# Kernel optimization log

Measured on AMD Instinct MI355X. Metric: run time of the kernel, lower is better.

Reference implementation:

```python
import jax, jax.numpy as jnp
import numpy as np

N = 50000; E = 800000; IN = 64; HID = 128; H = 8; C = 16; G = 64
NEG = 0.2  # leaky_relu negative slope (GATv2 default and explicit in forward)

def _ln(x, g, b, eps=1e-5):
    mu = jnp.mean(x, -1, keepdims=True)
    var = jnp.var(x, -1, keepdims=True)
    return (x - mu) * jax.lax.rsqrt(var + eps) * g + b

def _prelu(x, a):
    return jnp.where(x >= 0, x, a * x)

def _gatv2(h, src, dst, Wl, bl, Wr, br, att, bias):
    # GATv2Conv: heads=H, out=C per head, concat=True, add_self_loops=True
    n = h.shape[0]
    loop = jnp.arange(n, dtype=src.dtype)
    s = jnp.concatenate([src, loop]); d = jnp.concatenate([dst, loop])
    xl = (h @ Wl + bl).reshape(n, H, C)   # source transform (messages)
    xr = (h @ Wr + br).reshape(n, H, C)   # target transform
    z = jax.nn.leaky_relu(xl[s] + xr[d], NEG)          # [Etot,H,C]
    e = jnp.einsum('ehc,hc->eh', z, att)               # [Etot,H]
    m = jax.ops.segment_max(e, d, num_segments=n)      # scatter-softmax over dst
    w = jnp.exp(e - m[d])
    denom = jax.ops.segment_sum(w, d, num_segments=n)
    alpha = w / (denom[d] + 1e-16)
    out = jax.ops.segment_sum(xl[s] * alpha[:, :, None], d, num_segments=n)
    return out.reshape(n, H * C) + bias

def _sage(h, src, dst, Wp, bp, Wl, bl, Wr):
    # SAGEConv(aggr='mean', normalize=True, project=True)
    n = h.shape[0]
    xp = jax.nn.relu(h @ Wp + bp)                      # project before aggregation
    summ = jax.ops.segment_sum(xp[src], dst, num_segments=n)
    cnt = jax.ops.segment_sum(jnp.ones_like(dst, dtype=h.dtype), dst, num_segments=n)
    mean = summ / jnp.maximum(cnt, 1.0)[:, None]
    out = mean @ Wl + bl + h @ Wr                      # root uses un-projected h
    nrm = jnp.linalg.norm(out, axis=-1, keepdims=True)
    return out / jnp.maximum(nrm, 1e-12)               # F.normalize(p=2, dim=-1)

def _forward(x, W_in, b_in, W_res, b_res,
             g0_Wl, g0_bl, g0_Wr, g0_br, g0_att, g0_bias,
             s1_Wp, s1_bp, s1_Wl, s1_bl, s1_Wr,
             g2_Wl, g2_bl, g2_Wr, g2_br, g2_att, g2_bias,
             s3_Wp, s3_bp, s3_Wl, s3_bl, s3_Wr,
             ln_g, ln_b, Wap, bap,
             Wc1, bc1, a1, Wc2, bc2, a2, Wc3, bc3,
             edge_index, batch):
    src, dst = edge_index[0], edge_index[1]
    h = (x @ W_in + b_in) + (x @ W_res + b_res)        # input_proj + res_proj
    xs0 = jax.nn.elu(_ln(_gatv2(h, src, dst, g0_Wl, g0_bl, g0_Wr, g0_br, g0_att, g0_bias), ln_g[0], ln_b[0]))
    xs1 = jax.nn.leaky_relu(_ln(_sage(xs0, src, dst, s1_Wp, s1_bp, s1_Wl, s1_bl, s1_Wr), ln_g[1], ln_b[1]), NEG)
    xs2 = jax.nn.elu(_ln(_gatv2(xs1, src, dst, g2_Wl, g2_bl, g2_Wr, g2_br, g2_att, g2_bias), ln_g[2], ln_b[2]))
    xs3 = jax.nn.leaky_relu(_ln(_sage(xs2, src, dst, s3_Wp, s3_bp, s3_Wl, s3_bl, s3_Wr), ln_g[3], ln_b[3]), NEG)
    h = jnp.maximum(jnp.maximum(xs0, xs1), jnp.maximum(xs2, xs3))  # JumpingKnowledge('max')
    att = jax.nn.sigmoid(h @ Wap + bap)
    h = h * att
    summ = jax.ops.segment_sum(h, batch, num_segments=G)
    cnt = jax.ops.segment_sum(jnp.ones((h.shape[0],), h.dtype), batch, num_segments=G)
    pooled = summ / jnp.maximum(cnt, 1.0)[:, None]     # global_mean_pool
    z = _prelu(pooled @ Wc1 + bc1, a1)
    z = _prelu(z @ Wc2 + bc2, a2)
    return z @ Wc3 + bc3

def setup_inputs():
    key = jax.random.key(0)
    ks = iter(jax.random.split(key, 64))
    def nrm(shape, fan):
        return jax.random.normal(next(ks), shape, jnp.float32) / np.sqrt(fan).astype(np.float32)
    inp = {}
    inp['x'] = jax.random.normal(next(ks), (N, IN), jnp.float32)
    inp['edge_index'] = jax.random.randint(next(ks), (2, E), 0, N, jnp.int32)
    inp['batch'] = jnp.sort(jax.random.randint(next(ks), (N,), 0, G, jnp.int32))
    inp['W_in'] = nrm((IN, HID), IN); inp['b_in'] = jnp.zeros((HID,))
    inp['W_res'] = nrm((IN, HID), IN); inp['b_res'] = jnp.zeros((HID,))
    for p in ('g0', 'g2'):
        inp[p + '_Wl'] = nrm((HID, HID), HID); inp[p + '_bl'] = jnp.zeros((HID,))
        inp[p + '_Wr'] = nrm((HID, HID), HID); inp[p + '_br'] = jnp.zeros((HID,))
        inp[p + '_att'] = nrm((H, C), C); inp[p + '_bias'] = jnp.zeros((HID,))
    for p in ('s1', 's3'):
        inp[p + '_Wp'] = nrm((HID, HID), HID); inp[p + '_bp'] = jnp.zeros((HID,))
        inp[p + '_Wl'] = nrm((HID, HID), HID); inp[p + '_bl'] = jnp.zeros((HID,))
        inp[p + '_Wr'] = nrm((HID, HID), HID)
    inp['ln_g'] = jnp.ones((4, HID)); inp['ln_b'] = jnp.zeros((4, HID))
    inp['Wap'] = nrm((HID, 1), HID); inp['bap'] = jnp.zeros((1,))
    inp['Wc1'] = nrm((HID, HID), HID); inp['bc1'] = jnp.zeros((HID,))
    inp['a1'] = jnp.float32(0.25)
    inp['Wc2'] = nrm((HID, HID // 2), HID); inp['bc2'] = jnp.zeros((HID // 2,))
    inp['a2'] = jnp.float32(0.25)
    inp['Wc3'] = nrm((HID // 2, 2), HID // 2); inp['bc3'] = jnp.zeros((2,))
    return inp

def reference(x, edge_index, batch, W_in, b_in, W_res, b_res,
              g0_Wl, g0_bl, g0_Wr, g0_br, g0_att, g0_bias,
              s1_Wp, s1_bp, s1_Wl, s1_bl, s1_Wr,
              g2_Wl, g2_bl, g2_Wr, g2_br, g2_att, g2_bias,
              s3_Wp, s3_bp, s3_Wl, s3_bl, s3_Wr,
              ln_g, ln_b, Wap, bap, Wc1, bc1, a1, Wc2, bc2, a2, Wc3, bc3):
    return _forward(x, W_in, b_in, W_res, b_res,
                    g0_Wl, g0_bl, g0_Wr, g0_br, g0_att, g0_bias,
                    s1_Wp, s1_bp, s1_Wl, s1_bl, s1_Wr,
                    g2_Wl, g2_bl, g2_Wr, g2_br, g2_att, g2_bias,
                    s3_Wp, s3_bp, s3_Wl, s3_bl, s3_Wr,
                    ln_g, ln_b, Wap, bap, Wc1, bc1, a1, Wc2, bc2, a2, Wc3, bc3,
                    edge_index, batch)
```

## Files before the change

kernel.cpp:

```cpp
#include <hip/hip_runtime.h>
#include <math.h>

constexpr int N_ = 50000;
constexpr int E_ = 800000;
constexpr int IN_ = 64;
constexpr int HID_ = 128;
constexpr int G_ = 64;
constexpr float NEG_ = 0.2f;
constexpr float LOG2E_ = 1.44269504088896340736f;

#define ACT_NONE 0
#define ACT_RELU 1

typedef _Float16 half8 __attribute__((ext_vector_type(8)));
typedef _Float16 half2v __attribute__((ext_vector_type(2)));
typedef float floatx4 __attribute__((ext_vector_type(4)));

__global__ __launch_bounds__(256) void hist_kernel(const int* __restrict__ dst,
                                                   int* __restrict__ deg, int e) {
  int i = blockIdx.x * 256 + threadIdx.x;
  if (i < e) atomicAdd(&deg[dst[i]], 1);
}

__global__ __launch_bounds__(256) void scan1_kernel(const int* __restrict__ deg,
                                                    int* __restrict__ excl,
                                                    int* __restrict__ bscan, int n) {
  __shared__ int sh[256];
  int t = threadIdx.x;
  int i = blockIdx.x * 256 + t;
  int v = (i < n) ? deg[i] : 0;
  sh[t] = v;
  __syncthreads();
  for (int off = 1; off < 256; off <<= 1) {
    int y = (t >= off) ? sh[t - off] : 0;
    __syncthreads();
    sh[t] += y;
    __syncthreads();
  }
  int incl = sh[t];
  if (i < n) excl[i] = incl - v;
  if (t == 255) bscan[blockIdx.x] = incl;
}

__global__ __launch_bounds__(256) void scan2_kernel(int* __restrict__ data, int nb) {
  __shared__ int sh[256];
  int t = threadIdx.x;
  int v = (t < nb) ? data[t] : 0;
  sh[t] = v;
  __syncthreads();
  for (int off = 1; off < 256; off <<= 1) {
    int y = (t >= off) ? sh[t - off] : 0;
    __syncthreads();
    sh[t] += y;
    __syncthreads();
  }
  if (t < nb) data[t] = sh[t] - v;
}

__global__ __launch_bounds__(256) void scan3_kernel(int* __restrict__ rowptr,
                                                    int* __restrict__ cursor,
                                                    const int* __restrict__ bscan,
                                                    int n, int e) {
  int i = blockIdx.x * 256 + threadIdx.x;
  if (i < n) {
    int v = rowptr[i] + bscan[blockIdx.x];
    rowptr[i] = v;
    cursor[i] = v;
  }
  if (i == n) rowptr[n] = e;
}

__global__ __launch_bounds__(256) void fill_kernel(const int* __restrict__ src,
                                                   const int* __restrict__ dst,
                                                   int* __restrict__ cursor,
                                                   int* __restrict__ csr, int e) {
  int i = blockIdx.x * 256 + threadIdx.x;
  if (i < e) {
    int d = dst[i];
    int p = atomicAdd(&cursor[d], 1);
    csr[p] = src[i];
  }
}

__global__ __launch_bounds__(256) void addv_kernel(const float* __restrict__ a,
                                                   const float* __restrict__ b,
                                                   float* __restrict__ o, int n) {
  int i = blockIdx.x * 256 + threadIdx.x;
  if (i < n) o[i] = a[i] + b[i];
}

__global__ __launch_bounds__(256) void prep_w_kernel(
    const float* __restrict__ W_in, const float* __restrict__ W_res,
    const float* __restrict__ m0, const float* __restrict__ m1,
    const float* __restrict__ m2, const float* __restrict__ m3,
    const float* __restrict__ m4, const float* __restrict__ m5,
    const float* __restrict__ m6, const float* __restrict__ m7,
    const float* __restrict__ m8, const float* __restrict__ m9,
    _Float16* __restrict__ dst) {
  int idx = blockIdx.x * 256 + threadIdx.x;
  if (idx < 8192) {
    int n = idx >> 6, k = idx & 63;
    float v = W_in[k * 128 + n] + W_res[k * 128 + n];
    _Float16 h = (_Float16)v;
    dst[idx] = h;
    dst[8192 + idx] = (_Float16)(v - (float)h);
  } else if (idx < 8192 + 10 * 16384) {
    int r = idx - 8192;
    int j = r >> 14;
    int e = r & 16383;
    int n = e >> 7, k = e & 127;
    const float* S;
    switch (j) {
      case 0: S = m0; break; case 1: S = m1; break; case 2: S = m2; break;
      case 3: S = m3; break; case 4: S = m4; break; case 5: S = m5; break;
      case 6: S = m6; break; case 7: S = m7; break; case 8: S = m8; break;
      default: S = m9; break;
    }
    float v = S[k * 128 + n];
    _Float16 h = (_Float16)v;
    _Float16* base = dst + 16384 + j * 32768;
    base[e] = h;
    base[16384 + e] = (_Float16)(v - (float)h);
  }
}

__device__ inline void split8v(float4 a, float4 b, half8& h, half8& l) {
  float v0 = a.x, v1 = a.y, v2 = a.z, v3 = a.w;
  float v4 = b.x, v5 = b.y, v6 = b.z, v7 = b.w;
  _Float16 h0 = (_Float16)v0, h1 = (_Float16)v1, h2 = (_Float16)v2, h3 = (_Float16)v3;
  _Float16 h4 = (_Float16)v4, h5 = (_Float16)v5, h6 = (_Float16)v6, h7 = (_Float16)v7;
  h[0] = h0; h[1] = h1; h[2] = h2; h[3] = h3; h[4] = h4; h[5] = h5; h[6] = h6; h[7] = h7;
  l[0] = (_Float16)(v0 - (float)h0); l[1] = (_Float16)(v1 - (float)h1);
  l[2] = (_Float16)(v2 - (float)h2); l[3] = (_Float16)(v3 - (float)h3);
  l[4] = (_Float16)(v4 - (float)h4); l[5] = (_Float16)(v5 - (float)h5);
  l[6] = (_Float16)(v6 - (float)h6); l[7] = (_Float16)(v7 - (float)h7);
}


template <int K1, int ACT, typename OutT>
__global__ __launch_bounds__(256, 2) void gemm_rw(const float* __restrict__ A,
                                                  const _Float16* __restrict__ Wh,
                                                  const _Float16* __restrict__ Wl,
                                                  const float* __restrict__ bias,
                                                  OutT* __restrict__ C, int M) {
  constexpr int KK = K1 / 32;
  const int t = threadIdx.x;
  const int wave = t >> 6, lane = t & 63;
  const int quad = lane >> 4, l16 = lane & 15;
  const int nt0 = wave * 2;

  half8 wh[2][KK], wl[2][KK];
  float bb[2];
  int col[2];
#pragma unroll
  for (int i = 0; i < 2; ++i) {
    col[i] = (nt0 + i) * 16 + l16;
    bb[i] = bias[col[i]];
#pragma unroll
    for (int k = 0; k < KK; ++k) {
      size_t off = (size_t)col[i] * K1 + k * 32 + quad * 8;
      wh[i][k] = *reinterpret_cast<const half8*>(Wh + off);
      wl[i][k] = *reinterpret_cast<const half8*>(Wl + off);
    }
  }
  const int r0 = blockIdx.x * 64;
#pragma unroll
  for (int tt = 0; tt < 4; ++tt) {
    int tb = r0 + tt * 16;
    if (tb >= M) break;
    int arow = tb + l16;
    if (arow >= M) arow = M - 1;
    const float* ap = A + (size_t)arow * K1 + quad * 8;
    float4 a0[KK], a1[KK];
#pragma unroll
    for (int k = 0; k < KK; ++k) {
      a0[k] = *reinterpret_cast<const float4*>(ap + k * 32);
      a1[k] = *reinterpret_cast<const float4*>(ap + k * 32 + 4);
    }
    floatx4 acc[2];
    acc[0] = (floatx4){0.f, 0.f, 0.f, 0.f};
    acc[1] = (floatx4){0.f, 0.f, 0.f, 0.f};
#pragma unroll
    for (int k = 0; k < KK; ++k) {
      half8 ah, al;
      split8v(a0[k], a1[k], ah, al);
      acc[0] = __builtin_amdgcn_mfma_f32_16x16x32_f16(ah, wh[0][k], acc[0], 0, 0, 0);
      acc[0] = __builtin_amdgcn_mfma_f32_16x16x32_f16(ah, wl[0][k], acc[0], 0, 0, 0);
      acc[0] = __builtin_amdgcn_mfma_f32_16x16x32_f16(al, wh[0][k], acc[0], 0, 0, 0);
      acc[1] = __builtin_amdgcn_mfma_f32_16x16x32_f16(ah, wh[1][k], acc[1], 0, 0, 0);
      acc[1] = __builtin_amdgcn_mfma_f32_16x16x32_f16(ah, wl[1][k], acc[1], 0, 0, 0);
      acc[1] = __builtin_amdgcn_mfma_f32_16x16x32_f16(al, wh[1][k], acc[1], 0, 0, 0);
    }
#pragma unroll
    for (int i = 0; i < 2; ++i) {
#pragma unroll
      for (int reg = 0; reg < 4; ++reg) {
        int r = tb + quad * 4 + reg;
        if (r < M) {
          float v = acc[i][reg] + bb[i];
          if (ACT == ACT_RELU) v = fmaxf(v, 0.f);
          C[(size_t)r * 128 + col[i]] = (OutT)v;
        }
      }
    }
  }
}

__global__ __launch_bounds__(256, 2) void gemm_rw_dual_gat(const float* __restrict__ A,
                                                           const _Float16* __restrict__ W0h,
                                                           const _Float16* __restrict__ W0l,
                                                           const _Float16* __restrict__ W1h,
                                                           const _Float16* __restrict__ W1l,
                                                           const float* __restrict__ b0,
                                                           const float* __restrict__ b1,
                                                           _Float16* __restrict__ C0,
                                                           _Float16* __restrict__ C1, int M) {
  const int t = threadIdx.x;
  const int wave = t >> 6, lane = t & 63;
  const int quad = lane >> 4, l16 = lane & 15;
  const int nt0 = wave * 2;

  half8 w0h[2][4], w0l[2][4], w1h[2][4], w1l[2][4];
  float bb0[2], bb1[2];
  int col[2];
#pragma unroll
  for (int i = 0; i < 2; ++i) {
    col[i] = (nt0 + i) * 16 + l16;
    bb0[i] = b0[col[i]];
    bb1[i] = b1[col[i]];
#pragma unroll
    for (int k = 0; k < 4; ++k) {
      size_t off = (size_t)col[i] * 128 + k * 32 + quad * 8;
      w0h[i][k] = *reinterpret_cast<const half8*>(W0h + off);
      w0l[i][k] = *reinterpret_cast<const half8*>(W0l + off);
      w1h[i][k] = *reinterpret_cast<const half8*>(W1h + off);
      w1l[i][k] = *reinterpret_cast<const half8*>(W1l + off);
    }
  }
  const int r0 = blockIdx.x * 64;
#pragma unroll
  for (int tt = 0; tt < 4; ++tt) {
    int tb = r0 + tt * 16;
    if (tb >= M) break;
    int arow = tb + l16;
    if (arow >= M) arow = M - 1;
    const float* ap = A + (size_t)arow * 128 + quad * 8;
    float4 a0[4], a1[4];
#pragma unroll
    for (int k = 0; k < 4; ++k) {
      a0[k] = *reinterpret_cast<const float4*>(ap + k * 32);
      a1[k] = *reinterpret_cast<const float4*>(ap + k * 32 + 4);
    }
    floatx4 acc0[2], acc1[2];
    acc0[0] = (floatx4){0.f, 0.f, 0.f, 0.f};
    acc0[1] = (floatx4){0.f, 0.f, 0.f, 0.f};
    acc1[0] = (floatx4){0.f, 0.f, 0.f, 0.f};
    acc1[1] = (floatx4){0.f, 0.f, 0.f, 0.f};
#pragma unroll
    for (int k = 0; k < 4; ++k) {
      half8 ah, al;
      split8v(a0[k], a1[k], ah, al);
#pragma unroll
      for (int i = 0; i < 2; ++i) {
        acc0[i] = __builtin_amdgcn_mfma_f32_16x16x32_f16(ah, w0h[i][k], acc0[i], 0, 0, 0);
        acc0[i] = __builtin_amdgcn_mfma_f32_16x16x32_f16(ah, w0l[i][k], acc0[i], 0, 0, 0);
        acc0[i] = __builtin_amdgcn_mfma_f32_16x16x32_f16(al, w0h[i][k], acc0[i], 0, 0, 0);
        acc1[i] = __builtin_amdgcn_mfma_f32_16x16x32_f16(ah, w1h[i][k], acc1[i], 0, 0, 0);
        acc1[i] = __builtin_amdgcn_mfma_f32_16x16x32_f16(ah, w1l[i][k], acc1[i], 0, 0, 0);
        acc1[i] = __builtin_amdgcn_mfma_f32_16x16x32_f16(al, w1h[i][k], acc1[i], 0, 0, 0);
      }
    }
#pragma unroll
    for (int i = 0; i < 2; ++i) {
#pragma unroll
      for (int reg = 0; reg < 4; ++reg) {
        int r = tb + quad * 4 + reg;
        if (r < M) {
          C0[(size_t)r * 128 + col[i]] = (_Float16)(acc0[i][reg] + bb0[i]);
          C1[(size_t)r * 128 + col[i]] = (_Float16)(acc1[i][reg] + bb1[i]);
        }
      }
    }
  }
}

__global__ __launch_bounds__(256, 2) void gemm_rw_dual_sage(const float* __restrict__ A1,
                                                            const _Float16* __restrict__ W1h,
                                                            const _Float16* __restrict__ W1l,
                                                            const float* __restrict__ A2,
                                                            const _Float16* __restrict__ W2h,
                                                            const _Float16* __restrict__ W2l,
                                                            const float* __restrict__ bias,
                                                            const float* __restrict__ lng,
                                                            const float* __restrict__ lnb,
                                                            float* __restrict__ C, int M) {
  const int t = threadIdx.x;
  const int wave = t >> 6, lane = t & 63;
  const int quad = lane >> 4, l16 = lane & 15;
  const int nt0 = wave * 2;

  half8 w1h[2][4], w1l[2][4], w2h[2][4], w2l[2][4];
  float bb[2], gg[2], lb[2];
  int col[2];
#pragma unroll
  for (int i = 0; i < 2; ++i) {
    col[i] = (nt0 + i) * 16 + l16;
    bb[i] = bias[col[i]];
    gg[i] = lng[col[i]];
    lb[i] = lnb[col[i]];
#pragma unroll
    for (int k = 0; k < 4; ++k) {
      size_t off = (size_t)col[i] * 128 + k * 32 + quad * 8;
      w1h[i][k] = *reinterpret_cast<const half8*>(W1h + off);
      w1l[i][k] = *reinterpret_cast<const half8*>(W1l + off);
      w2h[i][k] = *reinterpret_cast<const half8*>(W2h + off);
      w2l[i][k] = *reinterpret_cast<const half8*>(W2l + off);
    }
  }
  __shared__ float2 red[2][4][16];
  const int r0 = blockIdx.x * 64;
#pragma unroll 1
  for (int tt = 0; tt < 4; ++tt) {
    int tb = r0 + tt * 16;
    if (tb >= M) break;
    int arow = tb + l16;
    if (arow >= M) arow = M - 1;
    const float* ap1 = A1 + (size_t)arow * 128 + quad * 8;
    const float* ap2 = A2 + (size_t)arow * 128 + quad * 8;
    float4 a0[4], a1[4], c0[4], c1[4];
#pragma unroll
    for (int k = 0; k < 4; ++k) {
      a0[k] = *reinterpret_cast<const float4*>(ap1 + k * 32);
      a1[k] = *reinterpret_cast<const float4*>(ap1 + k * 32 + 4);
      c0[k] = *reinterpret_cast<const float4*>(ap2 + k * 32);
      c1[k] = *reinterpret_cast<const float4*>(ap2 + k * 32 + 4);
    }
    floatx4 acc[2];
    acc[0] = (floatx4){0.f, 0.f, 0.f, 0.f};
    acc[1] = (floatx4){0.f, 0.f, 0.f, 0.f};
#pragma unroll
    for (int k = 0; k < 4; ++k) {
      half8 ah, al;
      split8v(a0[k], a1[k], ah, al);
#pragma unroll
      for (int i = 0; i < 2; ++i) {
        acc[i] = __builtin_amdgcn_mfma_f32_16x16x32_f16(ah, w1h[i][k], acc[i], 0, 0, 0);
        acc[i] = __builtin_amdgcn_mfma_f32_16x16x32_f16(ah, w1l[i][k], acc[i], 0, 0, 0);
        acc[i] = __builtin_amdgcn_mfma_f32_16x16x32_f16(al, w1h[i][k], acc[i], 0, 0, 0);
      }
    }
#pragma unroll
    for (int k = 0; k < 4; ++k) {
      half8 ah, al;
      split8v(c0[k], c1[k], ah, al);
#pragma unroll
      for (int i = 0; i < 2; ++i) {
        acc[i] = __builtin_amdgcn_mfma_f32_16x16x32_f16(ah, w2h[i][k], acc[i], 0, 0, 0);
        acc[i] = __builtin_amdgcn_mfma_f32_16x16x32_f16(ah, w2l[i][k], acc[i], 0, 0, 0);
        acc[i] = __builtin_amdgcn_mfma_f32_16x16x32_f16(al, w2h[i][k], acc[i], 0, 0, 0);
      }
    }
    float v0[4], v1[4], p1[4], p2[4];
#pragma unroll
    for (int reg = 0; reg < 4; ++reg) {
      v0[reg] = acc[0][reg] + bb[0];
      v1[reg] = acc[1][reg] + bb[1];
      p1[reg] = v0[reg] + v1[reg];
      p2[reg] = v0[reg] * v0[reg] + v1[reg] * v1[reg];
    }
#pragma unroll
    for (int off = 1; off < 16; off <<= 1) {
#pragma unroll
      for (int reg = 0; reg < 4; ++reg) {
        p1[reg] += __shfl_xor(p1[reg], off, 64);
        p2[reg] += __shfl_xor(p2[reg], off, 64);
      }
    }
    int par = tt & 1;
    if (l16 == 0) {
#pragma unroll
      for (int reg = 0; reg < 4; ++reg)
        red[par][wave][quad * 4 + reg] = make_float2(p1[reg], p2[reg]);
    }
    __syncthreads();
#pragma unroll
    for (int reg = 0; reg < 4; ++reg) {
      int rr = quad * 4 + reg;
      float2 q0 = red[par][0][rr], q1 = red[par][1][rr];
      float2 q2 = red[par][2][rr], q3 = red[par][3][rr];
      float s1 = q0.x + q1.x + q2.x + q3.x;
      float s2 = q0.y + q1.y + q2.y + q3.y;
      float inv = 1.f / fmaxf(sqrtf(s2), 1e-12f);
      float mu = s1 * inv * (1.f / 128.f);
      float ex2 = (s2 * inv) * inv * (1.f / 128.f);
      float rstd = rsqrtf(ex2 - mu * mu + 1e-5f);
      int r = tb + rr;
      if (r < M) {
        float o0 = (v0[reg] * inv - mu) * rstd * gg[0] + lb[0];
        float o1 = (v1[reg] * inv - mu) * rstd * gg[1] + lb[1];
        o0 = fmaxf(o0, NEG_ * o0);
        o1 = fmaxf(o1, NEG_ * o1);
        C[(size_t)r * 128 + col[0]] = o0;
        C[(size_t)r * 128 + col[1]] = o1;
      }
    }
  }
}

__global__ __launch_bounds__(256) void gat_ln_kernel(const _Float16* __restrict__ xl,
                                                     const _Float16* __restrict__ xr,
                                                     const float* __restrict__ att,
                                                     const float* __restrict__ gbias,
                                                     const int* __restrict__ rowptr,
                                                     const int* __restrict__ csr,
                                                     const float* __restrict__ lng,
                                                     const float* __restrict__ lnb,
                                                     float* __restrict__ out, int n) {
  int wid = (blockIdx.x * 256 + threadIdx.x) >> 6;
  int lane = threadIdx.x & 63;
  if (wid >= n) return;
  const half2v* __restrict__ xl2 = reinterpret_cast<const half2v*>(xl);
  const half2v xrv = reinterpret_cast<const half2v*>(xr)[wid * 64 + lane];
  float2 atv = reinterpret_cast<const float2*>(att)[lane];
  atv.x *= LOG2E_;
  atv.y *= LOG2E_;
  const half2v negc = {(_Float16)NEG_, (_Float16)NEG_};

  float m0, den;
  float2 acc;
  {
    half2v xv = xl2[wid * 64 + lane];
    half2v zz = xv + xrv;
    half2v zl = __builtin_elementwise_max(zz, zz * negc);
    float p = (float)zl[0] * atv.x + (float)zl[1] * atv.y;
    p += __shfl_xor(p, 1, 64);
    p += __shfl_xor(p, 2, 64);
    p += __shfl_xor(p, 4, 64);
    m0 = p;
    den = 1.f;
    acc = make_float2((float)xv[0], (float)xv[1]);
  }
  int beg = rowptr[wid], end = rowptr[wid + 1];
  for (int base = beg; base < end; base += 64) {
    int nb = end - base;
    if (nb > 64) nb = 64;
    int sl = (base + lane < end) ? csr[base + lane] : 0;
    int s0 = __builtin_amdgcn_readlane(sl, 0);
    half2v vbuf = xl2[s0 * 64 + lane];
    for (int j = 0; j < nb; ++j) {
      half2v xv = vbuf;
      if (j + 1 < nb) {
        int sn = __builtin_amdgcn_readlane(sl, j + 1);
        vbuf = xl2[sn * 64 + lane];
      }
      half2v zz = xv + xrv;
      half2v zl = __builtin_elementwise_max(zz, zz * negc);
      float p = (float)zl[0] * atv.x + (float)zl[1] * atv.y;
      p += __shfl_xor(p, 1, 64);
      p += __shfl_xor(p, 2, 64);
      p += __shfl_xor(p, 4, 64);
      float w = exp2f(p - m0);
      den += w;
      acc.x += w * (float)xv[0];
      acc.y += w * (float)xv[1];
    }
  }
  float inv = 1.f / (den + 1e-16f);
  const float2 bv = reinterpret_cast<const float2*>(gbias)[lane];
  float o0 = acc.x * inv + bv.x;
  float o1 = acc.y * inv + bv.y;
  float s1 = o0 + o1;
  float s2 = o0 * o0 + o1 * o1;
#pragma unroll
  for (int off = 1; off < 64; off <<= 1) {
    s1 += __shfl_xor(s1, off, 64);
    s2 += __shfl_xor(s2, off, 64);
  }
  float mu = s1 * (1.f / 128.f);
  float var = s2 * (1.f / 128.f) - mu * mu;
  float rstd = rsqrtf(var + 1e-5f);
  float2 gvv = reinterpret_cast<const float2*>(lng)[lane];
  float2 lbv = reinterpret_cast<const float2*>(lnb)[lane];
  float e0 = (o0 - mu) * rstd * gvv.x + lbv.x;
  float e1 = (o1 - mu) * rstd * gvv.y + lbv.y;
  e0 = e0 > 0.f ? e0 : exp2f(e0 * LOG2E_) - 1.f;
  e1 = e1 > 0.f ? e1 : exp2f(e1 * LOG2E_) - 1.f;
  reinterpret_cast<float2*>(out)[wid * 64 + lane] = make_float2(e0, e1);
}

__global__ __launch_bounds__(256) void sage_agg_kernel(const _Float16* __restrict__ xp,
                                                       const int* __restrict__ rowptr,
                                                       const int* __restrict__ csr,
                                                       float* __restrict__ mean, int n) {
  int wid = (blockIdx.x * 256 + threadIdx.x) >> 6;
  int lane = threadIdx.x & 63;
  if (wid >= n) return;
  const half2v* __restrict__ xp2 = reinterpret_cast<const half2v*>(xp);
  int beg = rowptr[wid], end = rowptr[wid + 1];
  float2 acc0 = make_float2(0.f, 0.f), acc1 = make_float2(0.f, 0.f);
  for (int base = beg; base < end; base += 64) {
    int nb = end - base;
    if (nb > 64) nb = 64;
    int sl = (base + lane < end) ? csr[base + lane] : 0;
    int j = 0;
    for (; j + 2 <= nb; j += 2) {
      int s0 = __builtin_amdgcn_readlane(sl, j);
      int s1i = __builtin_amdgcn_readlane(sl, j + 1);
      half2v v0 = xp2[s0 * 64 + lane];
      half2v v1 = xp2[s1i * 64 + lane];
      acc0.x += (float)v0[0]; acc0.y += (float)v0[1];
      acc1.x += (float)v1[0]; acc1.y += (float)v1[1];
    }
    if (j < nb) {
      int s0 = __builtin_amdgcn_readlane(sl, j);
      half2v v0 = xp2[s0 * 64 + lane];
      acc0.x += (float)v0[0]; acc0.y += (float)v0[1];
    }
  }
  float inv = 1.f / fmaxf((float)(end - beg), 1.f);
  float2 o = make_float2((acc0.x + acc1.x) * inv, (acc0.y + acc1.y) * inv);
  reinterpret_cast<float2*>(mean)[wid * 64 + lane] = o;
}

__global__ __launch_bounds__(256) void jk_pool_kernel(const float* __restrict__ x0,
                                                      const float* __restrict__ x1,
                                                      const float* __restrict__ x2,
                                                      const float* __restrict__ x3,
                                                      const float* __restrict__ wap,
                                                      const float* __restrict__ bap,
                                                      const int* __restrict__ batch,
                                                      float* __restrict__ pooled,
                                                      float* __restrict__ cnt, int n,
                                                      int chunk) {
  int wid = (blockIdx.x * 256 + threadIdx.x) >> 6;
  int lane = threadIdx.x & 63;
  int start = wid * chunk;
  if (start >= n) return;
  int end = start + chunk;
  if (end > n) end = n;

  const float2 wv = reinterpret_cast<const float2*>(wap)[lane];
  const float b0 = bap[0];

  int cur = -1;
  float2 acc = make_float2(0.f, 0.f);
  float c = 0.f;

  for (int i = start; i < end; ++i) {
    int off = i * 64 + lane;
    float2 a0 = reinterpret_cast<const float2*>(x0)[off];
    float2 a1 = reinterpret_cast<const float2*>(x1)[off];
    float2 a2 = reinterpret_cast<const float2*>(x2)[off];
    float2 a3 = reinterpret_cast<const float2*>(x3)[off];
    float2 v;
    v.x = fmaxf(fmaxf(a0.x, a1.x), fmaxf(a2.x, a3.x));
    v.y = fmaxf(fmaxf(a0.y, a1.y), fmaxf(a2.y, a3.y));
    float p = v.x * wv.x + v.y * wv.y;
#pragma unroll
    for (int o = 1; o < 64; o <<= 1) p += __shfl_xor(p, o, 64);
    float a = 1.f / (1.f + exp2f(-(p + b0) * LOG2E_));
    int bg = batch[i];
    if (bg != cur) {
      if (cur >= 0) {
        atomicAdd(&pooled[cur * 128 + 2 * lane], acc.x);
        atomicAdd(&pooled[cur * 128 + 2 * lane + 1], acc.y);
        if (lane == 0) atomicAdd(&cnt[cur], c);
      }
      cur = bg;
      acc = make_float2(0.f, 0.f);
      c = 0.f;
    }
    acc.x += v.x * a;
    acc.y += v.y * a;
    c += 1.f;
  }
  if (cur >= 0) {
    atomicAdd(&pooled[cur * 128 + 2 * lane], acc.x);
    atomicAdd(&pooled[cur * 128 + 2 * lane + 1], acc.y);
    if (lane == 0) atomicAdd(&cnt[cur], c);
  }
}

__global__ __launch_bounds__(128) void mlp_kernel(const float* __restrict__ pooled,
                                                  const float* __restrict__ cnt,
                                                  const float* __restrict__ Wc1,
                                                  const float* __restrict__ bc1,
                                                  const float* __restrict__ a1,
                                                  const float* __restrict__ Wc2,
                                                  const float* __restrict__ bc2,
                                                  const float* __restrict__ a2,
                                                  const float* __restrict__ Wc3,
                                                  const float* __restrict__ bc3,
                                                  float* __restrict__ out) {
  __shared__ float sh[128];
  __shared__ float sh2[128];
  __shared__ float sh3[64];
  int g = blockIdx.x, t = threadIdx.x;
  float inv = 1.f / fmaxf(cnt[g], 1.f);
  sh[t] = pooled[g * 128 + t] * inv;
  __syncthreads();
  float z = bc1[t];
  for (int k = 0; k < 128; ++k) z += sh[k] * Wc1[k * 128 + t];
  float al = a1[0];
  z = z >= 0.f ? z : al * z;
  sh2[t] = z;
  __syncthreads();
  if (t < 64) {
    float z2 = bc2[t];
    for (int k = 0; k < 128; ++k) z2 += sh2[k] * Wc2[k * 64 + t];
    float a2v = a2[0];
    z2 = z2 >= 0.f ? z2 : a2v * z2;
    sh3[t] = z2;
  }
  __syncthreads();
  if (t < 2) {
    float o = bc3[t];
    for (int k = 0; k < 64; ++k) o += sh3[k] * Wc3[k * 2 + t];
    out[g * 2 + t] = o;
  }
}

extern "C" void kernel_launch(void* const* d_in, const int* in_sizes, int n_in,
                              void* d_out, int out_size, void* d_ws, size_t ws_size,
                              hipStream_t stream) {
  const float* x = (const float*)d_in[0];
  const int* ei = (const int*)d_in[1];
  const int* batch = (const int*)d_in[2];
  const float* W_in = (const float*)d_in[3];
  const float* b_in = (const float*)d_in[4];
  const float* W_res = (const float*)d_in[5];
  const float* b_res = (const float*)d_in[6];
  const float* g0_Wl = (const float*)d_in[7];
  const float* g0_bl = (const float*)d_in[8];
  const float* g0_Wr = (const float*)d_in[9];
  const float* g0_br = (const float*)d_in[10];
  const float* g0_att = (const float*)d_in[11];
  const float* g0_bias = (const float*)d_in[12];
  const float* g2_Wl = (const float*)d_in[13];
  const float* g2_bl = (const float*)d_in[14];
  const float* g2_Wr = (const float*)d_in[15];
  const float* g2_br = (const float*)d_in[16];
  const float* g2_att = (const float*)d_in[17];
  const float* g2_bias = (const float*)d_in[18];
  const float* s1_Wp = (const float*)d_in[19];
  const float* s1_bp = (const float*)d_in[20];
  const float* s1_Wl = (const float*)d_in[21];
  const float* s1_bl = (const float*)d_in[22];
  const float* s1_Wr = (const float*)d_in[23];
  const float* s3_Wp = (const float*)d_in[24];
  const float* s3_bp = (const float*)d_in[25];
  const float* s3_Wl = (const float*)d_in[26];
  const float* s3_bl = (const float*)d_in[27];
  const float* s3_Wr = (const float*)d_in[28];
  const float* ln_g = (const float*)d_in[29];
  const float* ln_b = (const float*)d_in[30];
  const float* Wap = (const float*)d_in[31];
  const float* bap = (const float*)d_in[32];
  const float* Wc1 = (const float*)d_in[33];
  const float* bc1 = (const float*)d_in[34];
  const float* a1 = (const float*)d_in[35];
  const float* Wc2 = (const float*)d_in[36];
  const float* bc2 = (const float*)d_in[37];
  const float* a2 = (const float*)d_in[38];
  const float* Wc3 = (const float*)d_in[39];
  const float* bc3 = (const float*)d_in[40];
  float* out = (float*)d_out;

  char* w = (char*)d_ws;
  auto alloc = [&](size_t bytes) -> void* {
    void* p = (void*)w;
    w += (bytes + 255) & ~(size_t)255;
    return p;
  };
  int* deg_cursor = (int*)alloc((size_t)N_ * 4);
  int* rowptr = (int*)alloc((size_t)(N_ + 1) * 4);
  int* bscan = (int*)alloc(256 * 4);
  int* csr = (int*)alloc((size_t)E_ * 4);
  float* bsumf = (float*)alloc((size_t)HID_ * 4);
  float* pooled = (float*)alloc((size_t)G_ * HID_ * 4);
  float* cntf = (float*)alloc((size_t)G_ * 4);
  _Float16* wsp = (_Float16*)alloc((size_t)(16384 + 10 * 32768) * 2);
  size_t big = (size_t)N_ * HID_ * 4;
  size_t bigh = (size_t)N_ * HID_ * 2;
  float* T1 = (float*)alloc(big);
  float* T2 = (float*)alloc(big);
  _Float16* H0 = (_Float16*)alloc(bigh);
  _Float16* H1 = (_Float16*)alloc(bigh);
  float* B0 = (float*)alloc(big);
  float* B1 = (float*)alloc(big);
  float* B2 = (float*)alloc(big);
  float* B3 = (float*)alloc(big);

  const _Float16* WsT_h = wsp;
  const _Float16* WsT_l = wsp + 8192;
  auto WTh = [&](int j) { return (const _Float16*)(wsp + 16384 + j * 32768); };
  auto WTl = [&](int j) { return (const _Float16*)(wsp + 16384 + j * 32768 + 16384); };

  const int EB = (E_ + 255) / 256;
  const int NB256 = (N_ + 255) / 256;
  const int WB = (N_ + 3) / 4;
  const int GB = (N_ + 63) / 64;

  hipMemsetAsync(deg_cursor, 0, (size_t)N_ * 4, stream);
  hist_kernel<<<EB, 256, 0, stream>>>(ei + E_, deg_cursor, E_);
  scan1_kernel<<<NB256, 256, 0, stream>>>(deg_cursor, rowptr, bscan, N_);
  scan2_kernel<<<1, 256, 0, stream>>>(bscan, NB256);
  scan3_kernel<<<NB256, 256, 0, stream>>>(rowptr, deg_cursor, bscan, N_, E_);
  fill_kernel<<<EB, 256, 0, stream>>>(ei, ei + E_, deg_cursor, csr, E_);

  prep_w_kernel<<<(8192 + 10 * 16384 + 255) / 256, 256, 0, stream>>>(
      W_in, W_res, g0_Wl, g0_Wr, s1_Wp, s1_Wl, s1_Wr, g2_Wl, g2_Wr, s3_Wp, s3_Wl, s3_Wr, wsp);
  addv_kernel<<<1, 256, 0, stream>>>(b_in, b_res, bsumf, HID_);

  gemm_rw<64, ACT_NONE, float><<<GB, 256, 0, stream>>>(x, WsT_h, WsT_l, bsumf, T2, N_);

  gemm_rw_dual_gat<<<GB, 256, 0, stream>>>(T2, WTh(0), WTl(0), WTh(1), WTl(1), g0_bl, g0_br,
                                           H0, H1, N_);
  gat_ln_kernel<<<WB, 256, 0, stream>>>(H0, H1, g0_att, g0_bias, rowptr, csr,
                                        ln_g + 0 * 128, ln_b + 0 * 128, B0, N_);

  gemm_rw<128, ACT_RELU, _Float16><<<GB, 256, 0, stream>>>(B0, WTh(2), WTl(2), s1_bp, H0, N_);
  sage_agg_kernel<<<WB, 256, 0, stream>>>(H0, rowptr, csr, T1, N_);
  gemm_rw_dual_sage<<<GB, 256, 0, stream>>>(T1, WTh(3), WTl(3), B0, WTh(4), WTl(4), s1_bl,
                                            ln_g + 1 * 128, ln_b + 1 * 128, B1, N_);

  gemm_rw_dual_gat<<<GB, 256, 0, stream>>>(B1, WTh(5), WTl(5), WTh(6), WTl(6), g2_bl, g2_br,
                                           H0, H1, N_);
  gat_ln_kernel<<<WB, 256, 0, stream>>>(H0, H1, g2_att, g2_bias, rowptr, csr,
                                        ln_g + 2 * 128, ln_b + 2 * 128, B2, N_);

  gemm_rw<128, ACT_RELU, _Float16><<<GB, 256, 0, stream>>>(B2, WTh(7), WTl(7), s3_bp, H0, N_);
  sage_agg_kernel<<<WB, 256, 0, stream>>>(H0, rowptr, csr, T1, N_);
  gemm_rw_dual_sage<<<GB, 256, 0, stream>>>(T1, WTh(8), WTl(8), B2, WTh(9), WTl(9), s3_bl,
                                            ln_g + 3 * 128, ln_b + 3 * 128, B3, N_);

  hipMemsetAsync(pooled, 0, (size_t)G_ * HID_ * 4, stream);
  hipMemsetAsync(cntf, 0, (size_t)G_ * 4, stream);
  {
    const int chunk = 12;
    int nwaves = (N_ + chunk - 1) / chunk;
    int nblocks = (nwaves + 3) / 4;
    jk_pool_kernel<<<nblocks, 256, 0, stream>>>(B0, B1, B2, B3, Wap, bap, batch,
                                                pooled, cntf, N_, chunk);
  }
  mlp_kernel<<<G_, 128, 0, stream>>>(pooled, cntf, Wc1, bc1, a1, Wc2, bc2, a2, Wc3, bc3, out);
}
```

Measured before the change: 728.8 us.

## Process eight edges in parallel per wave in GAT and SAGE aggregation

Remaps the GAT and SAGE neighbor-aggregation kernels so each wave handles eight edges at once. Each lane covers one head or channel group of 16 channels, loaded as two half8 vectors, instead of the wave walking edges one at a time with two channels per lane. This removes the serial per-edge loop and the per-edge cross-lane shuffles for the attention score; partial sums are combined with an xor-shuffle reduction at the end. The trade-off is more registers per lane (16-element accumulators and attention weights), dynamic indexing of those arrays that could spill to scratch, and wasted lanes on low-degree tail chunks.

```diff
diff --git a/kernel.cpp b/kernel.cpp
--- a/kernel.cpp
+++ b/kernel.cpp
@@ -136,7 +136,6 @@
   l[6] = (_Float16)(v6 - (float)h6); l[7] = (_Float16)(v7 - (float)h7);
 }
 
-
 template <int K1, int ACT, typename OutT>
 __global__ __launch_bounds__(256, 2) void gemm_rw(const float* __restrict__ A,
                                                   const _Float16* __restrict__ Wh,
@@ -419,56 +418,79 @@
   int wid = (blockIdx.x * 256 + threadIdx.x) >> 6;
   int lane = threadIdx.x & 63;
   if (wid >= n) return;
-  const half2v* __restrict__ xl2 = reinterpret_cast<const half2v*>(xl);
-  const half2v xrv = reinterpret_cast<const half2v*>(xr)[wid * 64 + lane];
-  float2 atv = reinterpret_cast<const float2*>(att)[lane];
-  atv.x *= LOG2E_;
-  atv.y *= LOG2E_;
-  const half2v negc = {(_Float16)NEG_, (_Float16)NEG_};
+  const int h = lane >> 3, e = lane & 7;
+  const _Float16* __restrict__ xh = xl + h * 16;
+
+  const half8* xrp = reinterpret_cast<const half8*>(xr + (size_t)wid * 128 + h * 16);
+  half8 xr0 = xrp[0], xr1 = xrp[1];
+  float attf[16];
+#pragma unroll
+  for (int i = 0; i < 16; ++i) attf[i] = att[h * 16 + i] * LOG2E_;
+  const half8 negc = {(_Float16)NEG_, (_Float16)NEG_, (_Float16)NEG_, (_Float16)NEG_,
+                      (_Float16)NEG_, (_Float16)NEG_, (_Float16)NEG_, (_Float16)NEG_};
 
   float m0, den;
-  float2 acc;
+  float acc[16];
   {
-    half2v xv = xl2[wid * 64 + lane];
-    half2v zz = xv + xrv;
-    half2v zl = __builtin_elementwise_max(zz, zz * negc);
-    float p = (float)zl[0] * atv.x + (float)zl[1] * atv.y;
-    p += __shfl_xor(p, 1, 64);
-    p += __shfl_xor(p, 2, 64);
-    p += __shfl_xor(p, 4, 64);
+    const half8* sp = reinterpret_cast<const half8*>(xh + (size_t)wid * 128);
+    half8 s0 = sp[0], s1 = sp[1];
+    half8 z0 = s0 + xr0, z1 = s1 + xr1;
+    z0 = __builtin_elementwise_max(z0, z0 * negc);
+    z1 = __builtin_elementwise_max(z1, z1 * negc);
+    float p = 0.f;
+#pragma unroll
+    for (int i = 0; i < 8; ++i) {
+      p += (float)z0[i] * attf[i];
+      p += (float)z1[i] * attf[8 + i];
+    }
     m0 = p;
-    den = 1.f;
-    acc = make_float2((float)xv[0], (float)xv[1]);
-  }
+    float w = (e == 0) ? 1.f : 0.f;
+    den = w;
+#pragma unroll
+    for (int i = 0; i < 8; ++i) {
+      acc[i] = w * (float)s0[i];
+      acc[8 + i] = w * (float)s1[i];
+    }
+  }
+
   int beg = rowptr[wid], end = rowptr[wid + 1];
-  for (int base = beg; base < end; base += 64) {
-    int nb = end - base;
-    if (nb > 64) nb = 64;
-    int sl = (base + lane < end) ? csr[base + lane] : 0;
-    int s0 = __builtin_amdgcn_readlane(sl, 0);
-    half2v vbuf = xl2[s0 * 64 + lane];
-    for (int j = 0; j < nb; ++j) {
-      half2v xv = vbuf;
-      if (j + 1 < nb) {
-        int sn = __builtin_amdgcn_readlane(sl, j + 1);
-        vbuf = xl2[sn * 64 + lane];
-      }
-      half2v zz = xv + xrv;
-      half2v zl = __builtin_elementwise_max(zz, zz * negc);
-      float p = (float)zl[0] * atv.x + (float)zl[1] * atv.y;
-      p += __shfl_xor(p, 1, 64);
-      p += __shfl_xor(p, 2, 64);
-      p += __shfl_xor(p, 4, 64);
-      float w = exp2f(p - m0);
-      den += w;
-      acc.x += w * (float)xv[0];
-      acc.y += w * (float)xv[1];
-    }
-  }
+  for (int base = beg; base < end; base += 8) {
+    int idx = base + e;
+    bool valid = idx < end;
+    int ci = valid ? idx : end - 1;
+    int s = csr[ci];
+    const half8* gp = reinterpret_cast<const half8*>(xh + (size_t)s * 128);
+    half8 x0 = gp[0], x1 = gp[1];
+    half8 z0 = x0 + xr0, z1 = x1 + xr1;
+    z0 = __builtin_elementwise_max(z0, z0 * negc);
+    z1 = __builtin_elementwise_max(z1, z1 * negc);
+    float p = 0.f;
+#pragma unroll
+    for (int i = 0; i < 8; ++i) {
+      p += (float)z0[i] * attf[i];
+      p += (float)z1[i] * attf[8 + i];
+    }
+    float w = valid ? exp2f(p - m0) : 0.f;
+    den += w;
+#pragma unroll
+    for (int i = 0; i < 8; ++i) {
+      acc[i] += w * (float)x0[i];
+      acc[8 + i] += w * (float)x1[i];
+    }
+  }
+
+#pragma unroll
+  for (int off = 1; off < 8; off <<= 1) {
+    den += __shfl_xor(den, off, 64);
+#pragma unroll
+    for (int i = 0; i < 16; ++i) acc[i] += __shfl_xor(acc[i], off, 64);
+  }
+
   float inv = 1.f / (den + 1e-16f);
-  const float2 bv = reinterpret_cast<const float2*>(gbias)[lane];
-  float o0 = acc.x * inv + bv.x;
-  float o1 = acc.y * inv + bv.y;
+  int c = h * 16 + 2 * e;
+  float2 bv = reinterpret_cast<const float2*>(gbias + c)[0];
+  float o0 = acc[2 * e] * inv + bv.x;
+  float o1 = acc[2 * e + 1] * inv + bv.y;
   float s1 = o0 + o1;
   float s2 = o0 * o0 + o1 * o1;
 #pragma unroll
@@ -479,13 +501,13 @@
   float mu = s1 * (1.f / 128.f);
   float var = s2 * (1.f / 128.f) - mu * mu;
   float rstd = rsqrtf(var + 1e-5f);
-  float2 gvv = reinterpret_cast<const float2*>(lng)[lane];
-  float2 lbv = reinterpret_cast<const float2*>(lnb)[lane];
+  float2 gvv = reinterpret_cast<const float2*>(lng + c)[0];
+  float2 lbv = reinterpret_cast<const float2*>(lnb + c)[0];
   float e0 = (o0 - mu) * rstd * gvv.x + lbv.x;
   float e1 = (o1 - mu) * rstd * gvv.y + lbv.y;
   e0 = e0 > 0.f ? e0 : exp2f(e0 * LOG2E_) - 1.f;
   e1 = e1 > 0.f ? e1 : exp2f(e1 * LOG2E_) - 1.f;
-  reinterpret_cast<float2*>(out)[wid * 64 + lane] = make_float2(e0, e1);
+  *reinterpret_cast<float2*>(out + (size_t)wid * 128 + c) = make_float2(e0, e1);
 }
 
 __global__ __launch_bounds__(256) void sage_agg_kernel(const _Float16* __restrict__ xp,
@@ -495,31 +517,37 @@
   int wid = (blockIdx.x * 256 + threadIdx.x) >> 6;
   int lane = threadIdx.x & 63;
   if (wid >= n) return;
-  const half2v* __restrict__ xp2 = reinterpret_cast<const half2v*>(xp);
+  const int g = lane >> 3, e = lane & 7;
+  const _Float16* __restrict__ xg = xp + g * 16;
+
+  float acc[16];
+#pragma unroll
+  for (int i = 0; i < 16; ++i) acc[i] = 0.f;
+
   int beg = rowptr[wid], end = rowptr[wid + 1];
-  float2 acc0 = make_float2(0.f, 0.f), acc1 = make_float2(0.f, 0.f);
-  for (int base = beg; base < end; base += 64) {
-    int nb = end - base;
-    if (nb > 64) nb = 64;
-    int sl = (base + lane < end) ? csr[base + lane] : 0;
-    int j = 0;
-    for (; j + 2 <= nb; j += 2) {
-      int s0 = __builtin_amdgcn_readlane(sl, j);
-      int s1i = __builtin_amdgcn_readlane(sl, j + 1);
-      half2v v0 = xp2[s0 * 64 + lane];
-      half2v v1 = xp2[s1i * 64 + lane];
-      acc0.x += (float)v0[0]; acc0.y += (float)v0[1];
-      acc1.x += (float)v1[0]; acc1.y += (float)v1[1];
-    }
-    if (j < nb) {
-      int s0 = __builtin_amdgcn_readlane(sl, j);
-      half2v v0 = xp2[s0 * 64 + lane];
-      acc0.x += (float)v0[0]; acc0.y += (float)v0[1];
-    }
+  for (int base = beg; base < end; base += 8) {
+    int idx = base + e;
+    bool valid = idx < end;
+    int ci = valid ? idx : end - 1;
+    int s = csr[ci];
+    const half8* gp = reinterpret_cast<const half8*>(xg + (size_t)s * 128);
+    half8 x0 = gp[0], x1 = gp[1];
+    float w = valid ? 1.f : 0.f;
+#pragma unroll
+    for (int i = 0; i < 8; ++i) {
+      acc[i] += w * (float)x0[i];
+      acc[8 + i] += w * (float)x1[i];
+    }
+  }
+#pragma unroll
+  for (int off = 1; off < 8; off <<= 1) {
+#pragma unroll
+    for (int i = 0; i < 16; ++i) acc[i] += __shfl_xor(acc[i], off, 64);
   }
   float inv = 1.f / fmaxf((float)(end - beg), 1.f);
-  float2 o = make_float2((acc0.x + acc1.x) * inv, (acc0.y + acc1.y) * inv);
-  reinterpret_cast<float2*>(mean)[wid * 64 + lane] = o;
+  int c = g * 16 + 2 * e;
+  *reinterpret_cast<float2*>(mean + (size_t)wid * 128 + c) =
+      make_float2(acc[2 * e] * inv, acc[2 * e + 1] * inv);
 }
 
 __global__ __launch_bounds__(256) void jk_pool_kernel(const float* __restrict__ x0,
```

Result: no change. 720.7 us (-1.1%).
